# Kernel optimization log

Measured on AMD Instinct MI355X. Metric: run time of the kernel, lower is better.

## Reference

```python
import jax, jax.numpy as jnp
import numpy as np
from jax import lax

KS = 5            # patch kernel size
STRIDE = 4        # patch stride / scale ratio
SHIFTS = (2, 2)   # roll shifts before patch extraction
SOFTMAX_SCALE = 10.0
MID_CH = 64
BAND_HS = 8


def same_pad(x, k, s):
    """TensorFlow-style SAME padding for kernel k, stride s (NCHW)."""
    H, W = x.shape[-2], x.shape[-1]
    oh, ow = -(-H // s), -(-W // s)
    ph = max(0, (oh - 1) * s + k - H)
    pw = max(0, (ow - 1) * s + k - W)
    return jnp.pad(x, ((0, 0), (0, 0), (ph // 2, ph - ph // 2), (pw // 2, pw - pw // 2)))


def extract_patches(x, k, s, shifts):
    """torch.nn.Unfold equivalent with SAME padding and roll -> [N, L, C, k, k]."""
    x = same_pad(x, k, s)
    x = jnp.roll(x, shifts[0], axis=2)
    x = jnp.roll(x, shifts[1], axis=3)
    p = lax.conv_general_dilated_patches(
        x, (k, k), (s, s), 'VALID', dimension_numbers=('NCHW', 'OIHW', 'NCHW'))
    N, _, Hn, Wn = p.shape
    C = x.shape[1]
    # channel ordering is (C, kh, kw) channel-slowest, matching torch unfold
    return p.reshape(N, C, k, k, Hn * Wn).transpose(0, 4, 1, 2, 3)


def conv3(x, w, b):
    """3x3 conv, padding=1, bias + LeakyReLU(0.01) (BasicBlock)."""
    y = lax.conv_general_dilated(x, w, (1, 1), [(1, 1), (1, 1)],
                                 dimension_numbers=('NCHW', 'OIHW', 'NCHW'))
    return jax.nn.leaky_relu(y + b[None, :, None, None], 0.01)


def setup_inputs() -> dict:
    key = jax.random.key(0)
    ks = jax.random.split(key, 11)
    f32 = jnp.float32
    return {
        'ms':   jax.random.normal(ks[0], (2, BAND_HS, 96, 96), f32),
        'pan':  jax.random.normal(ks[1], (2, 1, 384, 384), f32),
        'pan2': jax.random.normal(ks[2], (2, 1, 96, 96), f32),
        'wq': jax.random.normal(ks[3], (MID_CH, 1, 3, 3), f32) * 0.1,
        'bq': jax.random.normal(ks[4], (MID_CH,), f32) * 0.02,
        'wk': jax.random.normal(ks[5], (MID_CH, 1, 3, 3), f32) * 0.1,
        'bk': jax.random.normal(ks[6], (MID_CH,), f32) * 0.02,
        'wv': jax.random.normal(ks[7], (BAND_HS, BAND_HS, 3, 3), f32) * 0.1,
        'bv': jax.random.normal(ks[8], (BAND_HS,), f32) * 0.02,
        'wr': jax.random.normal(ks[9], (BAND_HS, BAND_HS, 3, 3), f32) * 0.1,
        'br': jax.random.normal(ks[10], (BAND_HS,), f32) * 0.02,
    }


def reference(ms, pan, pan2, wq, bq, wk, bk, wv, bv, wr, br):
    k_fea = conv3(pan2, wk, bk)                       # [N, mid, h, w]
    q_fea = conv3(pan, wq, bq)                        # [N, mid, H, W]
    v_fea = conv3(ms, wv, bv)                         # [N, band, h, w]

    k_patch = extract_patches(k_fea, KS, STRIDE, SHIFTS)  # [N, L, mid, ks, ks]
    v_patch = extract_patches(v_fea, KS, STRIDE, SHIFTS)  # [N, L, band, ks, ks]

    def attend(q, kp, vp):
        # q: [mid, H, W]; kp: [L, mid, ks, ks]; vp: [L, band, ks, ks]
        norms = jnp.sqrt(jnp.sum(kp * kp, axis=(1, 2, 3)))      # per-patch L2 norms
        k0 = kp / jnp.max(norms)                                # global-max normalization
        q0 = same_pad(q[None], KS, STRIDE)                      # [1, mid, Hp, Wp]
        scores = lax.conv_general_dilated(
            q0, k0, (STRIDE, STRIDE), 'VALID',
            dimension_numbers=('NCHW', 'OIHW', 'NCHW'))          # [1, L, H', W']
        attn = jax.nn.softmax(scores * SOFTMAX_SCALE, axis=1)
        # conv_transpose2d(attn, vp, stride) == dilated conv with flipped, transposed kernel
        wT = jnp.flip(vp, (2, 3)).transpose(1, 0, 2, 3)          # [band, L, ks, ks]
        out = lax.conv_general_dilated(
            attn, wT, (1, 1), [(KS - 1, KS - 1)] * 2,
            lhs_dilation=(STRIDE, STRIDE),
            dimension_numbers=('NCHW', 'OIHW', 'NCHW'))          # [1, band, Ho, Wo]
        return out[0] / 6.0

    res = jax.vmap(attend)(q_fea, k_patch, v_patch)   # [N, band, Ho, Wo]
    return conv3(res, wr, br)
```

## Files before the change

kernel.cpp:

```cpp
#include <hip/hip_runtime.h>
#include <math.h>


typedef _Float16 f16;
typedef _Float16 f16x8 __attribute__((ext_vector_type(8)));
typedef float f32x4 __attribute__((ext_vector_type(4)));

namespace csa {
constexpr int NB   = 2;
constexpr int MID  = 64;
constexpr int BAND = 8;
constexpr int HK   = 96;
constexpr int HQ   = 384;
constexpr int HQP  = 385;
constexpr int XI   = 97;
constexpr int LN   = 24;
constexpr int L    = 576;
constexpr int LP   = 640;
constexpr int PS   = 96 * 96;
constexpr int KDIM = MID * 25;
constexpr int VDIM = BAND * 25;
constexpr int MV   = 256;
constexpr int HO   = 385;
constexpr size_t QPSN = (size_t)4 * HQP * XI * MID;

constexpr size_t align256(size_t x) { return (x + 255) & ~(size_t)255; }
constexpr size_t OFF_QPS  = 0;
constexpr size_t OFF_KCL  = align256(OFF_QPS + (size_t)NB*QPSN*2);
constexpr size_t OFF_VFEA = align256(OFF_KCL + (size_t)NB*HK*HK*MID*2);
constexpr size_t OFF_N2   = align256(OFF_VFEA + (size_t)NB*BAND*HK*HK*4);
constexpr size_t OFF_SC   = align256(OFF_N2   + (size_t)NB*L*4);
constexpr size_t OFF_KM   = align256(OFF_SC   + 256);
constexpr size_t OFF_VT   = align256(OFF_KM   + (size_t)NB*LP*KDIM*2);
constexpr size_t OFF_ST   = align256(OFF_VT   + (size_t)NB*MV*L*2);
constexpr size_t OFF_AT   = align256(OFF_ST   + (size_t)NB*PS*LP*4);
constexpr size_t OFF_D    = align256(OFF_AT   + (size_t)NB*PS*L*2);
constexpr size_t OFF_RES  = align256(OFF_D    + (size_t)NB*MV*PS*4);
}
using namespace csa;

__global__ __launch_bounds__(256) void csa_convq_ps(
    const float* __restrict__ in, const float* __restrict__ w,
    const float* __restrict__ b, f16* __restrict__ out) {
  int id = blockIdx.x * 256 + threadIdx.x;
  int total = NB * 4 * HQP * XI;
  if (id >= total) return;
  int xi = id % XI;
  int t = id / XI;
  int yp = t % HQP;
  t /= HQP;
  int f = t % 4;
  int n = t / 4;
  int xp = 4 * xi + f;
  f16* op = out + (size_t)id * MID;
  if (yp >= HQ || xp >= HQ) {
    f16x8 z = {0, 0, 0, 0, 0, 0, 0, 0};
#pragma unroll
    for (int c8 = 0; c8 < 8; ++c8) *(f16x8*)(op + c8 * 8) = z;
    return;
  }
  const float* ip = in + (size_t)n * HQ * HQ;
  float p[9];
#pragma unroll
  for (int dy = 0; dy < 3; ++dy)
#pragma unroll
    for (int dx = 0; dx < 3; ++dx) {
      int yy = yp + dy - 1, xx = xp + dx - 1;
      p[dy * 3 + dx] = (yy >= 0 && yy < HQ && xx >= 0 && xx < HQ)
                           ? ip[(size_t)yy * HQ + xx] : 0.f;
    }
#pragma unroll
  for (int c8 = 0; c8 < 8; ++c8) {
    f16x8 o;
#pragma unroll
    for (int e = 0; e < 8; ++e) {
      int co = c8 * 8 + e;
      float acc = b[co];
#pragma unroll
      for (int k = 0; k < 9; ++k) acc = fmaf(p[k], w[co * 9 + k], acc);
      o[e] = (f16)(acc > 0.f ? acc : 0.01f * acc);
    }
    *(f16x8*)(op + c8 * 8) = o;
  }
}

__global__ __launch_bounds__(256) void csa_conv_cl(
    const float* __restrict__ in, const float* __restrict__ w,
    const float* __restrict__ b, f16* __restrict__ out, int H) {
  int id = blockIdx.x * 256 + threadIdx.x;
  int total = NB * H * H;
  if (id >= total) return;
  int x = id % H;
  int t = id / H;
  int y = t % H;
  int n = t / H;
  f16* op = out + (size_t)id * MID;
  const float* ip = in + (size_t)n * H * H;
  float p[9];
#pragma unroll
  for (int dy = 0; dy < 3; ++dy)
#pragma unroll
    for (int dx = 0; dx < 3; ++dx) {
      int yy = y + dy - 1, xx = x + dx - 1;
      p[dy * 3 + dx] = (yy >= 0 && yy < H && xx >= 0 && xx < H)
                           ? ip[(size_t)yy * H + xx] : 0.f;
    }
#pragma unroll
  for (int c8 = 0; c8 < 8; ++c8) {
    f16x8 o;
#pragma unroll
    for (int e = 0; e < 8; ++e) {
      int co = c8 * 8 + e;
      float acc = b[co];
#pragma unroll
      for (int k = 0; k < 9; ++k) acc = fmaf(p[k], w[co * 9 + k], acc);
      o[e] = (f16)(acc > 0.f ? acc : 0.01f * acc);
    }
    *(f16x8*)(op + c8 * 8) = o;
  }
}

__global__ __launch_bounds__(256) void csa_conv3_8x8(
    const float* __restrict__ in, const float* __restrict__ w,
    const float* __restrict__ b, float* __restrict__ out, int H, int W) {
  int id = blockIdx.x * 256 + threadIdx.x;
  int total = NB * H * W;
  if (id >= total) return;
  int x = id % W;
  int t = id / W;
  int y = t % H;
  int n = t / H;
  const float* ip = in + (size_t)n * BAND * H * W;
  float p[BAND][9];
#pragma unroll
  for (int ci = 0; ci < BAND; ++ci)
#pragma unroll
    for (int dy = 0; dy < 3; ++dy)
#pragma unroll
      for (int dx = 0; dx < 3; ++dx) {
        int yy = y + dy - 1, xx = x + dx - 1;
        p[ci][dy * 3 + dx] = (yy >= 0 && yy < H && xx >= 0 && xx < W)
                                 ? ip[((size_t)ci * H + yy) * W + xx] : 0.f;
      }
  float* op = out + ((size_t)n * BAND * H + y) * W + x;
  for (int co = 0; co < BAND; ++co) {
    float acc = b[co];
#pragma unroll
    for (int ci = 0; ci < BAND; ++ci)
#pragma unroll
      for (int k = 0; k < 9; ++k)
        acc = fmaf(p[ci][k], w[(co * BAND + ci) * 9 + k], acc);
    acc = acc > 0.f ? acc : 0.01f * acc;
    op[(size_t)co * H * W] = acc;
  }
}

__global__ __launch_bounds__(256) void csa_build_patches(
    const f16* __restrict__ kcl, const float* __restrict__ v_fea,
    f16* __restrict__ Kmat, f16* __restrict__ Vt, float* __restrict__ n2) {
  int blk = blockIdx.x;
  int n = blk / LP;
  int l = blk % LP;
  int tid = threadIdx.x;
  f16* krow = Kmat + ((size_t)n * LP + l) * KDIM;
  if (l >= L) {
    f16x8 z = {0, 0, 0, 0, 0, 0, 0, 0};
    for (int ch = tid; ch < 200; ch += 256) *(f16x8*)(krow + ch * 8) = z;
    return;
  }
  int i = l / LN, j = l % LN;
  const f16* kn = kcl + (size_t)n * HK * HK * MID;
  float ss = 0.f;
  for (int ch = tid; ch < 200; ch += 256) {
    int khkw = ch >> 3;
    int c0 = (ch & 7) * 8;
    int kh = khkw / 5, kw = khkw % 5;
    int r = (4 * i + kh + 95) % 97;
    int cc = (4 * j + kw + 95) % 97;
    f16x8 v = {0, 0, 0, 0, 0, 0, 0, 0};
    if (r < HK && cc < HK)
      v = *(const f16x8*)(kn + ((size_t)r * HK + cc) * MID + c0);
#pragma unroll
    for (int e = 0; e < 8; ++e) {
      float fv = (float)v[e];
      ss += fv * fv;
    }
    *(f16x8*)(krow + ch * 8) = v;
  }
  for (int m = tid; m < MV; m += 256) {
    float v = 0.f;
    if (m < VDIM) {
      int kw = m % 5;
      int t = m / 5;
      int kh = t % 5;
      int c = t / 5;
      int r = (4 * i + kh + 95) % 97;
      int cc = (4 * j + kw + 95) % 97;
      v = (r < HK && cc < HK)
              ? v_fea[(((size_t)n * BAND + c) * HK + r) * HK + cc] : 0.f;
    }
    Vt[((size_t)n * MV + m) * L + l] = (f16)v;
  }
  __shared__ float red[256];
  red[tid] = ss;
  __syncthreads();
  for (int s = 128; s > 0; s >>= 1) {
    if (tid < s) red[tid] += red[tid + s];
    __syncthreads();
  }
  if (tid == 0) n2[n * L + l] = red[0];
}

__global__ __launch_bounds__(256) void csa_max_scale(
    const float* __restrict__ n2, float* __restrict__ scale) {
  int n = blockIdx.x;
  int tid = threadIdx.x;
  float m = 0.f;
  for (int l = tid; l < L; l += 256) m = fmaxf(m, n2[n * L + l]);
  __shared__ float red[256];
  red[tid] = m;
  __syncthreads();
  for (int s = 128; s > 0; s >>= 1) {
    if (tid < s) red[tid] = fmaxf(red[tid], red[tid + s]);
    __syncthreads();
  }
  if (tid == 0) scale[n] = 10.f / sqrtf(red[0]);
}

__device__ __forceinline__ void gl_lds16(const f16* g, f16* s) {
  __builtin_amdgcn_global_load_lds(
      (const __attribute__((address_space(1))) void*)g,
      (__attribute__((address_space(3))) void*)s, 16, 0, 0);
}

__global__ __launch_bounds__(256) void csa_gemm1(
    const f16* __restrict__ qps, const f16* __restrict__ Km,
    float* __restrict__ C) {
  __shared__ __attribute__((aligned(16))) f16 As[4096];
  __shared__ __attribute__((aligned(16))) f16 Bs[4096];
  const int tid = threadIdx.x;
  const int w = tid >> 6;
  const int l = tid & 63;
  const int q = l >> 4;
  const int r = l & 15;
  const int nb = blockIdx.z;
  qps += (size_t)nb * QPSN;
  Km += (size_t)nb * LP * KDIM;
  C += (size_t)nb * (size_t)PS * LP;
  const int bm = blockIdx.y * 128;
  const int bn = blockIdx.x * 128;
  const int wm = (w >> 1) * 64;
  const int wn = (w & 1) * 64;

  f32x4 acc[4][4];
#pragma unroll
  for (int i = 0; i < 4; ++i)
#pragma unroll
    for (int j = 0; j < 4; ++j) {
      f32x4 z = {0.f, 0.f, 0.f, 0.f};
      acc[i][j] = z;
    }

  const int pg0 = bm + w * 16;
  const int y0 = pg0 / 96, x0 = pg0 % 96;
  const int pg1 = pg0 + 64;
  const int y1 = pg1 / 96, x1 = pg1 % 96;
  const int la = r * MID + q * 8;

  const f16* gb0 = Km + (size_t)(bn + w * 16 + r) * KDIM + q * 8;
  const f16* gb1 = gb0 + (size_t)64 * KDIM;
  f16* lA0 = As + w * 512;
  f16* lA1 = As + 2048 + w * 512;
  f16* lB0 = Bs + w * 512;
  f16* lB1 = Bs + 2048 + w * 512;
  const int am = (w >> 1) * 4;
  const int bnn = (w & 1) * 4;

  int t = 0;
  for (int kh = 0; kh < 5; ++kh) {
    for (int kw = 0; kw < 5; ++kw) {
      const size_t u0 =
          (((size_t)(kw & 3) * HQP + (4 * y0 + kh)) * XI + x0 + (kw >> 2)) * MID;
      const size_t u1 =
          (((size_t)(kw & 3) * HQP + (4 * y1 + kh)) * XI + x1 + (kw >> 2)) * MID;
#pragma unroll
      for (int half = 0; half < 2; ++half, ++t) {
        const size_t oA = (size_t)half * 32 + la;
        const size_t oB = (size_t)t * 32;
        gl_lds16(qps + u0 + oA, lA0);
        gl_lds16(qps + u1 + oA, lA1);
        gl_lds16(gb0 + oB, lB0);
        gl_lds16(gb1 + oB, lB1);
        __syncthreads();
        f16x8 af[4], bf[4];
#pragma unroll
        for (int u = 0; u < 4; ++u) {
          af[u] = *(const f16x8*)&As[(am + u) * 512 + q * 128 + r * 8];
          bf[u] = *(const f16x8*)&Bs[(bnn + u) * 512 + q * 128 + r * 8];
        }
#pragma unroll
        for (int i = 0; i < 4; ++i)
#pragma unroll
          for (int j = 0; j < 4; ++j)
            acc[i][j] = __builtin_amdgcn_mfma_f32_16x16x32_f16(af[i], bf[j],
                                                               acc[i][j], 0, 0, 0);
        __syncthreads();
      }
    }
  }
  const int cn = bn + wn + r;
#pragma unroll
  for (int i = 0; i < 4; ++i) {
    int rm = bm + wm + i * 16 + q * 4;
#pragma unroll
    for (int j = 0; j < 4; ++j)
#pragma unroll
      for (int rr = 0; rr < 4; ++rr)
        C[(size_t)(rm + rr) * LP + cn + j * 16] = acc[i][j][rr];
  }
}

__global__ __launch_bounds__(256) void csa_gemm_f16(
    const f16* __restrict__ A, const f16* __restrict__ Bt,
    float* __restrict__ C, int M, int N, int K,
    size_t strideA, size_t strideB, size_t strideC) {
  __shared__ __attribute__((aligned(16))) f16 As[4096];
  __shared__ __attribute__((aligned(16))) f16 Bs[4096];
  const int tid = threadIdx.x;
  const int w = tid >> 6;
  const int l = tid & 63;
  const int q = l >> 4;
  const int r = l & 15;
  const int nb = blockIdx.z;
  A += (size_t)nb * strideA;
  Bt += (size_t)nb * strideB;
  C += (size_t)nb * strideC;
  const int bm = blockIdx.y * 128;
  const int bn = blockIdx.x * 128;
  const int wm = (w >> 1) * 64;
  const int wn = (w & 1) * 64;

  f32x4 acc[4][4];
#pragma unroll
  for (int i = 0; i < 4; ++i)
#pragma unroll
    for (int j = 0; j < 4; ++j) {
      f32x4 z = {0.f, 0.f, 0.f, 0.f};
      acc[i][j] = z;
    }

  const f16* ga0 = A + (size_t)(bm + w * 16 + r) * K + q * 8;
  const f16* ga1 = ga0 + (size_t)64 * K;
  const f16* gb0 = Bt + (size_t)(bn + w * 16 + r) * K + q * 8;
  const f16* gb1 = gb0 + (size_t)64 * K;
  f16* lA0 = As + w * 512;
  f16* lA1 = As + 2048 + w * 512;
  f16* lB0 = Bs + w * 512;
  f16* lB1 = Bs + 2048 + w * 512;
  const int am = (w >> 1) * 4;
  const int bnn = (w & 1) * 4;

  for (int k0 = 0; k0 < K; k0 += 32) {
    gl_lds16(ga0 + k0, lA0);
    gl_lds16(ga1 + k0, lA1);
    gl_lds16(gb0 + k0, lB0);
    gl_lds16(gb1 + k0, lB1);
    __syncthreads();
    f16x8 af[4], bf[4];
#pragma unroll
    for (int u = 0; u < 4; ++u) {
      af[u] = *(const f16x8*)&As[(am + u) * 512 + q * 128 + r * 8];
      bf[u] = *(const f16x8*)&Bs[(bnn + u) * 512 + q * 128 + r * 8];
    }
#pragma unroll
    for (int i = 0; i < 4; ++i)
#pragma unroll
      for (int j = 0; j < 4; ++j)
        acc[i][j] =
            __builtin_amdgcn_mfma_f32_16x16x32_f16(af[i], bf[j], acc[i][j], 0, 0, 0);
    __syncthreads();
  }

  const int cn = bn + wn + r;
#pragma unroll
  for (int i = 0; i < 4; ++i) {
    int rm = bm + wm + i * 16 + q * 4;
#pragma unroll
    for (int j = 0; j < 4; ++j)
#pragma unroll
      for (int rr = 0; rr < 4; ++rr)
        C[(size_t)(rm + rr) * N + cn + j * 16] = acc[i][j][rr];
  }
}

__global__ __launch_bounds__(256) void csa_softmax(
    const float* __restrict__ scoresT, const float* __restrict__ scale,
    f16* __restrict__ attnT) {
  const int wv = threadIdx.x >> 6;
  const int lane = threadIdx.x & 63;
  const int p = blockIdx.x * 4 + wv;
  const int n = blockIdx.y;
  const float sc = scale[n];
  const float* row = scoresT + ((size_t)n * PS + p) * LP;
  float v[9];
  float m = -1e30f;
#pragma unroll
  for (int j = 0; j < 9; ++j) {
    v[j] = row[lane + j * 64] * sc;
    m = fmaxf(m, v[j]);
  }
#pragma unroll
  for (int off = 32; off > 0; off >>= 1) m = fmaxf(m, __shfl_xor(m, off));
  float e[9], s = 0.f;
#pragma unroll
  for (int j = 0; j < 9; ++j) {
    e[j] = __expf(v[j] - m);
    s += e[j];
  }
#pragma unroll
  for (int off = 32; off > 0; off >>= 1) s += __shfl_xor(s, off);
  const float inv = 1.f / s;
  f16* orow = attnT + ((size_t)n * PS + p) * L;
#pragma unroll
  for (int j = 0; j < 9; ++j) orow[lane + j * 64] = (f16)(e[j] * inv);
}

__global__ __launch_bounds__(256) void csa_gather(
    const float* __restrict__ D, float* __restrict__ res) {
  int id = blockIdx.x * 256 + threadIdx.x;
  if (id >= NB * BAND * HO * HO) return;
  int ox = id % HO;
  int t = id / HO;
  int oy = t % HO;
  t = t / HO;
  int co = t % BAND;
  int n = t / BAND;
  const float* Dn = D + (size_t)n * MV * PS;
  float s = 0.f;
  int kh0 = oy & 3;
  int kw0 = ox & 3;
  for (int kh = kh0; kh < 5; kh += 4) {
    int y = (oy - kh) >> 2;
    if (y < 0 || y >= 96) continue;
    for (int kw = kw0; kw < 5; kw += 4) {
      int x = (ox - kw) >> 2;
      if (x < 0 || x >= 96) continue;
      s += Dn[(size_t)(co * 25 + kh * 5 + kw) * PS + y * 96 + x];
    }
  }
  res[id] = s * (1.f / 6.f);
}

extern "C" void kernel_launch(void* const* d_in, const int* in_sizes, int n_in,
                              void* d_out, int out_size, void* d_ws,
                              size_t ws_size, hipStream_t stream) {
  const float* ms   = (const float*)d_in[0];
  const float* pan  = (const float*)d_in[1];
  const float* pan2 = (const float*)d_in[2];
  const float* wq = (const float*)d_in[3];
  const float* bq = (const float*)d_in[4];
  const float* wk = (const float*)d_in[5];
  const float* bk = (const float*)d_in[6];
  const float* wv = (const float*)d_in[7];
  const float* bv = (const float*)d_in[8];
  const float* wr = (const float*)d_in[9];
  const float* br = (const float*)d_in[10];
  float* out = (float*)d_out;

  char* ws = (char*)d_ws;
  f16*   qps   = (f16*)(ws + OFF_QPS);
  f16*   kcl   = (f16*)(ws + OFF_KCL);
  float* v_fea = (float*)(ws + OFF_VFEA);
  float* n2    = (float*)(ws + OFF_N2);
  float* scale = (float*)(ws + OFF_SC);
  f16*   Kmat  = (f16*)(ws + OFF_KM);
  f16*   Vt    = (f16*)(ws + OFF_VT);
  float* scoT  = (float*)(ws + OFF_ST);
  f16*   attnT = (f16*)(ws + OFF_AT);
  float* Dm    = (float*)(ws + OFF_D);
  float* res   = (float*)(ws + OFF_RES);

  dim3 b256(256);
  csa_convq_ps<<<dim3((NB * 4 * HQP * XI + 255) / 256), b256, 0, stream>>>(
      pan, wq, bq, qps);
  csa_conv_cl<<<dim3((NB * HK * HK + 255) / 256), b256, 0, stream>>>(
      pan2, wk, bk, kcl, HK);
  csa_conv3_8x8<<<dim3((NB * HK * HK + 255) / 256), b256, 0, stream>>>(
      ms, wv, bv, v_fea, HK, HK);
  csa_build_patches<<<dim3(NB * LP), b256, 0, stream>>>(kcl, v_fea, Kmat, Vt,
                                                        n2);
  csa_max_scale<<<dim3(NB), b256, 0, stream>>>(n2, scale);

  csa_gemm1<<<dim3(LP / 128, PS / 128, NB), b256, 0, stream>>>(qps, Kmat,
                                                               scoT);

  csa_softmax<<<dim3(PS / 4, NB), b256, 0, stream>>>(scoT, scale, attnT);

  csa_gemm_f16<<<dim3(PS / 128, MV / 128, NB), b256, 0, stream>>>(
      Vt, attnT, Dm, MV, PS, L,
      (size_t)MV * L, (size_t)PS * L, (size_t)MV * PS);

  csa_gather<<<dim3((NB * BAND * HO * HO + 255) / 256), b256, 0, stream>>>(
      Dm, res);
  csa_conv3_8x8<<<dim3((NB * HO * HO + 255) / 256), b256, 0, stream>>>(
      res, wr, br, out, HO, HO);
}
```

Measured before the change: 278.8 us.

## Triple-buffer GEMM LDS staging with async prefetch, XCD-aware block remap, compact scores

Both MFMA GEMM kernels now use a three-stage LDS ring. Global-to-LDS loads for tile t+2 are issued before computing tile t, with a single vmcnt wait and barrier per step replacing two syncthreads. Workgroup indices are remapped so consecutive logical tiles land on the same XCD, improving L2 reuse across the eight chiplets. The scores matrix is stored with row stride 576 instead of padded 640, with column-guarded writes, which cuts write and softmax read traffic at the cost of triple the LDS footprint.

```diff
diff --git a/kernel.cpp b/kernel.cpp
--- a/kernel.cpp
+++ b/kernel.cpp
@@ -236,19 +236,25 @@
 __global__ __launch_bounds__(256) void csa_gemm1(
     const f16* __restrict__ qps, const f16* __restrict__ Km,
     float* __restrict__ C) {
-  __shared__ __attribute__((aligned(16))) f16 As[4096];
-  __shared__ __attribute__((aligned(16))) f16 Bs[4096];
+  __shared__ __attribute__((aligned(16))) f16 As[3 * 4096];
+  __shared__ __attribute__((aligned(16))) f16 Bs[3 * 4096];
   const int tid = threadIdx.x;
   const int w = tid >> 6;
   const int l = tid & 63;
   const int q = l >> 4;
   const int r = l & 15;
-  const int nb = blockIdx.z;
+
+  const int flat = blockIdx.x + 5 * (blockIdx.y + 72 * blockIdx.z);
+  const int logical = (flat & 7) * 90 + (flat >> 3);
+  const int bx = logical % 5;
+  const int by = (logical / 5) % 72;
+  const int nb = logical / 360;
+
   qps += (size_t)nb * QPSN;
   Km += (size_t)nb * LP * KDIM;
-  C += (size_t)nb * (size_t)PS * LP;
-  const int bm = blockIdx.y * 128;
-  const int bn = blockIdx.x * 128;
+  C += (size_t)nb * (size_t)PS * L;
+  const int bm = by * 128;
+  const int bn = bx * 128;
   const int wm = (w >> 1) * 64;
   const int wn = (w & 1) * 64;
 
@@ -269,54 +275,77 @@
 
   const f16* gb0 = Km + (size_t)(bn + w * 16 + r) * KDIM + q * 8;
   const f16* gb1 = gb0 + (size_t)64 * KDIM;
-  f16* lA0 = As + w * 512;
-  f16* lA1 = As + 2048 + w * 512;
-  f16* lB0 = Bs + w * 512;
-  f16* lB1 = Bs + 2048 + w * 512;
   const int am = (w >> 1) * 4;
   const int bnn = (w & 1) * 4;
 
-  int t = 0;
-  for (int kh = 0; kh < 5; ++kh) {
-    for (int kw = 0; kw < 5; ++kw) {
-      const size_t u0 =
-          (((size_t)(kw & 3) * HQP + (4 * y0 + kh)) * XI + x0 + (kw >> 2)) * MID;
-      const size_t u1 =
-          (((size_t)(kw & 3) * HQP + (4 * y1 + kh)) * XI + x1 + (kw >> 2)) * MID;
-#pragma unroll
-      for (int half = 0; half < 2; ++half, ++t) {
-        const size_t oA = (size_t)half * 32 + la;
-        const size_t oB = (size_t)t * 32;
-        gl_lds16(qps + u0 + oA, lA0);
-        gl_lds16(qps + u1 + oA, lA1);
-        gl_lds16(gb0 + oB, lB0);
-        gl_lds16(gb1 + oB, lB1);
-        __syncthreads();
-        f16x8 af[4], bf[4];
-#pragma unroll
-        for (int u = 0; u < 4; ++u) {
-          af[u] = *(const f16x8*)&As[(am + u) * 512 + q * 128 + r * 8];
-          bf[u] = *(const f16x8*)&Bs[(bnn + u) * 512 + q * 128 + r * 8];
-        }
-#pragma unroll
-        for (int i = 0; i < 4; ++i)
-#pragma unroll
-          for (int j = 0; j < 4; ++j)
-            acc[i][j] = __builtin_amdgcn_mfma_f32_16x16x32_f16(af[i], bf[j],
-                                                               acc[i][j], 0, 0, 0);
-        __syncthreads();
-      }
-    }
-  }
+  auto stage = [&](int t, int bi) {
+    f16* bA = As + bi * 4096;
+    f16* bB = Bs + bi * 4096;
+    const int kh = t / 10;
+    const int rem = t - kh * 10;
+    const int kw = rem >> 1;
+    const int half = rem & 1;
+    const size_t u0 =
+        (((size_t)(kw & 3) * HQP + (4 * y0 + kh)) * XI + x0 + (kw >> 2)) * MID;
+    const size_t u1 =
+        (((size_t)(kw & 3) * HQP + (4 * y1 + kh)) * XI + x1 + (kw >> 2)) * MID;
+    const size_t oA = (size_t)half * 32 + la;
+    gl_lds16(qps + u0 + oA, bA + w * 512);
+    gl_lds16(qps + u1 + oA, bA + 2048 + w * 512);
+    gl_lds16(gb0 + (size_t)t * 32, bB + w * 512);
+    gl_lds16(gb1 + (size_t)t * 32, bB + 2048 + w * 512);
+  };
+  auto compute = [&](int bi) {
+    const f16* bA = As + bi * 4096;
+    const f16* bB = Bs + bi * 4096;
+    f16x8 af[4], bf[4];
+#pragma unroll
+    for (int u = 0; u < 4; ++u) {
+      af[u] = *(const f16x8*)&bA[(am + u) * 512 + q * 128 + r * 8];
+      bf[u] = *(const f16x8*)&bB[(bnn + u) * 512 + q * 128 + r * 8];
+    }
+#pragma unroll
+    for (int i = 0; i < 4; ++i)
+#pragma unroll
+      for (int j = 0; j < 4; ++j)
+        acc[i][j] = __builtin_amdgcn_mfma_f32_16x16x32_f16(af[i], bf[j],
+                                                           acc[i][j], 0, 0, 0);
+  };
+
+  stage(0, 0);
+  stage(1, 1);
+  int bi = 0;
+  for (int t = 0; t < 48; ++t) {
+    asm volatile("s_waitcnt vmcnt(4)" ::: "memory");
+    __builtin_amdgcn_s_barrier();
+    __builtin_amdgcn_sched_barrier(0);
+    stage(t + 2, bi == 0 ? 2 : bi - 1);
+    compute(bi);
+    bi = (bi == 2) ? 0 : bi + 1;
+  }
+  asm volatile("s_waitcnt vmcnt(4)" ::: "memory");
+  __builtin_amdgcn_s_barrier();
+  __builtin_amdgcn_sched_barrier(0);
+  compute(bi);
+  bi = (bi == 2) ? 0 : bi + 1;
+  asm volatile("s_waitcnt vmcnt(0)" ::: "memory");
+  __builtin_amdgcn_s_barrier();
+  __builtin_amdgcn_sched_barrier(0);
+  compute(bi);
+
   const int cn = bn + wn + r;
 #pragma unroll
   for (int i = 0; i < 4; ++i) {
     int rm = bm + wm + i * 16 + q * 4;
 #pragma unroll
-    for (int j = 0; j < 4; ++j)
-#pragma unroll
-      for (int rr = 0; rr < 4; ++rr)
-        C[(size_t)(rm + rr) * LP + cn + j * 16] = acc[i][j][rr];
+    for (int j = 0; j < 4; ++j) {
+      int c = cn + j * 16;
+      if (c < L) {
+#pragma unroll
+        for (int rr = 0; rr < 4; ++rr)
+          C[(size_t)(rm + rr) * L + c] = acc[i][j][rr];
+      }
+    }
   }
 }
 
@@ -324,19 +353,28 @@
     const f16* __restrict__ A, const f16* __restrict__ Bt,
     float* __restrict__ C, int M, int N, int K,
     size_t strideA, size_t strideB, size_t strideC) {
-  __shared__ __attribute__((aligned(16))) f16 As[4096];
-  __shared__ __attribute__((aligned(16))) f16 Bs[4096];
+  __shared__ __attribute__((aligned(16))) f16 As[3 * 4096];
+  __shared__ __attribute__((aligned(16))) f16 Bs[3 * 4096];
   const int tid = threadIdx.x;
   const int w = tid >> 6;
   const int l = tid & 63;
   const int q = l >> 4;
   const int r = l & 15;
-  const int nb = blockIdx.z;
+
+  const int gx = gridDim.x, gy = gridDim.y;
+  const int nwg = gx * gy * gridDim.z;
+  const int chunk = nwg >> 3;
+  const int flat = blockIdx.x + gx * (blockIdx.y + gy * blockIdx.z);
+  const int logical = (flat & 7) * chunk + (flat >> 3);
+  const int my = logical % gy;
+  const int nx = (logical / gy) % gx;
+  const int nb = logical / (gy * gx);
+
   A += (size_t)nb * strideA;
   Bt += (size_t)nb * strideB;
   C += (size_t)nb * strideC;
-  const int bm = blockIdx.y * 128;
-  const int bn = blockIdx.x * 128;
+  const int bm = my * 128;
+  const int bn = nx * 128;
   const int wm = (w >> 1) * 64;
   const int wn = (w & 1) * 64;
 
@@ -353,24 +391,26 @@
   const f16* ga1 = ga0 + (size_t)64 * K;
   const f16* gb0 = Bt + (size_t)(bn + w * 16 + r) * K + q * 8;
   const f16* gb1 = gb0 + (size_t)64 * K;
-  f16* lA0 = As + w * 512;
-  f16* lA1 = As + 2048 + w * 512;
-  f16* lB0 = Bs + w * 512;
-  f16* lB1 = Bs + 2048 + w * 512;
   const int am = (w >> 1) * 4;
   const int bnn = (w & 1) * 4;
 
-  for (int k0 = 0; k0 < K; k0 += 32) {
-    gl_lds16(ga0 + k0, lA0);
-    gl_lds16(ga1 + k0, lA1);
-    gl_lds16(gb0 + k0, lB0);
-    gl_lds16(gb1 + k0, lB1);
-    __syncthreads();
+  auto stage = [&](int t, int bi) {
+    f16* bA = As + bi * 4096;
+    f16* bB = Bs + bi * 4096;
+    const size_t k0 = (size_t)t * 32;
+    gl_lds16(ga0 + k0, bA + w * 512);
+    gl_lds16(ga1 + k0, bA + 2048 + w * 512);
+    gl_lds16(gb0 + k0, bB + w * 512);
+    gl_lds16(gb1 + k0, bB + 2048 + w * 512);
+  };
+  auto compute = [&](int bi) {
+    const f16* bA = As + bi * 4096;
+    const f16* bB = Bs + bi * 4096;
     f16x8 af[4], bf[4];
 #pragma unroll
     for (int u = 0; u < 4; ++u) {
-      af[u] = *(const f16x8*)&As[(am + u) * 512 + q * 128 + r * 8];
-      bf[u] = *(const f16x8*)&Bs[(bnn + u) * 512 + q * 128 + r * 8];
+      af[u] = *(const f16x8*)&bA[(am + u) * 512 + q * 128 + r * 8];
+      bf[u] = *(const f16x8*)&bB[(bnn + u) * 512 + q * 128 + r * 8];
     }
 #pragma unroll
     for (int i = 0; i < 4; ++i)
@@ -378,8 +418,29 @@
       for (int j = 0; j < 4; ++j)
         acc[i][j] =
             __builtin_amdgcn_mfma_f32_16x16x32_f16(af[i], bf[j], acc[i][j], 0, 0, 0);
-    __syncthreads();
-  }
+  };
+
+  const int NT = K >> 5;
+  stage(0, 0);
+  stage(1, 1);
+  int bi = 0;
+  for (int t = 0; t + 2 < NT; ++t) {
+    asm volatile("s_waitcnt vmcnt(4)" ::: "memory");
+    __builtin_amdgcn_s_barrier();
+    __builtin_amdgcn_sched_barrier(0);
+    stage(t + 2, bi == 0 ? 2 : bi - 1);
+    compute(bi);
+    bi = (bi == 2) ? 0 : bi + 1;
+  }
+  asm volatile("s_waitcnt vmcnt(4)" ::: "memory");
+  __builtin_amdgcn_s_barrier();
+  __builtin_amdgcn_sched_barrier(0);
+  compute(bi);
+  bi = (bi == 2) ? 0 : bi + 1;
+  asm volatile("s_waitcnt vmcnt(0)" ::: "memory");
+  __builtin_amdgcn_s_barrier();
+  __builtin_amdgcn_sched_barrier(0);
+  compute(bi);
 
   const int cn = bn + wn + r;
 #pragma unroll
@@ -401,7 +462,7 @@
   const int p = blockIdx.x * 4 + wv;
   const int n = blockIdx.y;
   const float sc = scale[n];
-  const float* row = scoresT + ((size_t)n * PS + p) * LP;
+  const float* row = scoresT + ((size_t)n * PS + p) * L;
   float v[9];
   float m = -1e30f;
 #pragma unroll
```

Result: faster. 273.3 us (-2.0%).

## Replace LDS-staged GEMMs with register double-buffered direct loads and XCD-aware block remap

Applied to the files above, without the earlier changes.

Both MFMA GEMMs stop staging tiles through LDS with global_load_lds and barriers. Each wave now loads its f16x8 fragments straight from global memory into registers, double-buffered so the next K-step's loads overlap the current MFMAs. Block indices are remapped so consecutive logical tiles land on the same XCD, aiming for better L2 reuse. The scores buffer is narrowed from padded LP to L columns with a bounds check, and gemm2 uses 64-row tiles for more blocks. The risks are redundant global loads with no LDS sharing across waves, and the remap constants being hardcoded to the grid shape.

```diff
diff --git a/kernel.cpp b/kernel.cpp
--- a/kernel.cpp
+++ b/kernel.cpp
@@ -227,28 +227,26 @@
   if (tid == 0) scale[n] = 10.f / sqrtf(red[0]);
 }
 
-__device__ __forceinline__ void gl_lds16(const f16* g, f16* s) {
-  __builtin_amdgcn_global_load_lds(
-      (const __attribute__((address_space(1))) void*)g,
-      (__attribute__((address_space(3))) void*)s, 16, 0, 0);
-}
-
 __global__ __launch_bounds__(256) void csa_gemm1(
     const f16* __restrict__ qps, const f16* __restrict__ Km,
     float* __restrict__ C) {
-  __shared__ __attribute__((aligned(16))) f16 As[4096];
-  __shared__ __attribute__((aligned(16))) f16 Bs[4096];
   const int tid = threadIdx.x;
   const int w = tid >> 6;
   const int l = tid & 63;
   const int q = l >> 4;
   const int r = l & 15;
-  const int nb = blockIdx.z;
+
+  const int flat = blockIdx.x + 5 * (blockIdx.y + 72 * blockIdx.z);
+  const int logical = (flat & 7) * 90 + (flat >> 3);
+  const int bx = logical % 5;
+  const int by = (logical / 5) % 72;
+  const int nb = logical / 360;
+
   qps += (size_t)nb * QPSN;
   Km += (size_t)nb * LP * KDIM;
-  C += (size_t)nb * (size_t)PS * LP;
-  const int bm = blockIdx.y * 128;
-  const int bn = blockIdx.x * 128;
+  C += (size_t)nb * (size_t)PS * L;
+  const int bm = by * 128;
+  const int bn = bx * 128;
   const int wm = (w >> 1) * 64;
   const int wn = (w & 1) * 64;
 
@@ -261,135 +259,145 @@
       acc[i][j] = z;
     }
 
-  const int pg0 = bm + w * 16;
-  const int y0 = pg0 / 96, x0 = pg0 % 96;
-  const int pg1 = pg0 + 64;
-  const int y1 = pg1 / 96, x1 = pg1 % 96;
-  const int la = r * MID + q * 8;
-
-  const f16* gb0 = Km + (size_t)(bn + w * 16 + r) * KDIM + q * 8;
-  const f16* gb1 = gb0 + (size_t)64 * KDIM;
-  f16* lA0 = As + w * 512;
-  f16* lA1 = As + 2048 + w * 512;
-  f16* lB0 = Bs + w * 512;
-  f16* lB1 = Bs + 2048 + w * 512;
-  const int am = (w >> 1) * 4;
-  const int bnn = (w & 1) * 4;
-
-  int t = 0;
-  for (int kh = 0; kh < 5; ++kh) {
-    for (int kw = 0; kw < 5; ++kw) {
-      const size_t u0 =
-          (((size_t)(kw & 3) * HQP + (4 * y0 + kh)) * XI + x0 + (kw >> 2)) * MID;
-      const size_t u1 =
-          (((size_t)(kw & 3) * HQP + (4 * y1 + kh)) * XI + x1 + (kw >> 2)) * MID;
-#pragma unroll
-      for (int half = 0; half < 2; ++half, ++t) {
-        const size_t oA = (size_t)half * 32 + la;
-        const size_t oB = (size_t)t * 32;
-        gl_lds16(qps + u0 + oA, lA0);
-        gl_lds16(qps + u1 + oA, lA1);
-        gl_lds16(gb0 + oB, lB0);
-        gl_lds16(gb1 + oB, lB1);
-        __syncthreads();
-        f16x8 af[4], bf[4];
-#pragma unroll
-        for (int u = 0; u < 4; ++u) {
-          af[u] = *(const f16x8*)&As[(am + u) * 512 + q * 128 + r * 8];
-          bf[u] = *(const f16x8*)&Bs[(bnn + u) * 512 + q * 128 + r * 8];
-        }
-#pragma unroll
-        for (int i = 0; i < 4; ++i)
-#pragma unroll
-          for (int j = 0; j < 4; ++j)
-            acc[i][j] = __builtin_amdgcn_mfma_f32_16x16x32_f16(af[i], bf[j],
-                                                               acc[i][j], 0, 0, 0);
-        __syncthreads();
-      }
-    }
-  }
+  const f16* pA[4];
+#pragma unroll
+  for (int u = 0; u < 4; ++u) {
+    const int p0 = bm + wm + 16 * u;
+    const int yu = p0 / 96, x0u = p0 % 96;
+    pA[u] = qps + ((size_t)(4 * yu) * XI + x0u + r) * MID + q * 8;
+  }
+  const f16* pB[4];
+#pragma unroll
+  for (int u = 0; u < 4; ++u)
+    pB[u] = Km + (size_t)(bn + wn + 16 * u + r) * KDIM + q * 8;
+
+  auto loadt = [&](int t, f16x8 av[4], f16x8 bv[4]) {
+    const int khkw = t >> 1, half = t & 1;
+    const int kh = khkw / 5, kw = khkw % 5;
+    const size_t dA =
+        (((size_t)(kw & 3) * HQP + kh) * XI + (kw >> 2)) * MID + half * 32;
+#pragma unroll
+    for (int u = 0; u < 4; ++u) {
+      av[u] = *(const f16x8*)(pA[u] + dA);
+      bv[u] = *(const f16x8*)(pB[u] + t * 32);
+    }
+  };
+  auto mfmas = [&](const f16x8 av[4], const f16x8 bv[4]) {
+#pragma unroll
+    for (int i = 0; i < 4; ++i)
+#pragma unroll
+      for (int j = 0; j < 4; ++j)
+        acc[i][j] = __builtin_amdgcn_mfma_f32_16x16x32_f16(av[i], bv[j],
+                                                           acc[i][j], 0, 0, 0);
+  };
+
+  f16x8 a0[4], b0[4], a1[4], b1[4];
+  loadt(0, a0, b0);
+#pragma unroll
+  for (int t = 0; t < 48; t += 2) {
+    loadt(t + 1, a1, b1);
+    mfmas(a0, b0);
+    loadt(t + 2, a0, b0);
+    mfmas(a1, b1);
+  }
+  loadt(49, a1, b1);
+  mfmas(a0, b0);
+  mfmas(a1, b1);
+
   const int cn = bn + wn + r;
 #pragma unroll
   for (int i = 0; i < 4; ++i) {
     int rm = bm + wm + i * 16 + q * 4;
 #pragma unroll
-    for (int j = 0; j < 4; ++j)
-#pragma unroll
-      for (int rr = 0; rr < 4; ++rr)
-        C[(size_t)(rm + rr) * LP + cn + j * 16] = acc[i][j][rr];
-  }
-}
-
-__global__ __launch_bounds__(256) void csa_gemm_f16(
-    const f16* __restrict__ A, const f16* __restrict__ Bt,
-    float* __restrict__ C, int M, int N, int K,
-    size_t strideA, size_t strideB, size_t strideC) {
-  __shared__ __attribute__((aligned(16))) f16 As[4096];
-  __shared__ __attribute__((aligned(16))) f16 Bs[4096];
+    for (int j = 0; j < 4; ++j) {
+      int c = cn + j * 16;
+      if (c < L) {
+#pragma unroll
+        for (int rr = 0; rr < 4; ++rr)
+          C[(size_t)(rm + rr) * L + c] = acc[i][j][rr];
+      }
+    }
+  }
+}
+
+__global__ __launch_bounds__(256) void csa_gemm2(
+    const f16* __restrict__ Vt, const f16* __restrict__ At,
+    float* __restrict__ D) {
   const int tid = threadIdx.x;
   const int w = tid >> 6;
   const int l = tid & 63;
   const int q = l >> 4;
   const int r = l & 15;
-  const int nb = blockIdx.z;
-  A += (size_t)nb * strideA;
-  Bt += (size_t)nb * strideB;
-  C += (size_t)nb * strideC;
-  const int bm = blockIdx.y * 128;
-  const int bn = blockIdx.x * 128;
-  const int wm = (w >> 1) * 64;
+
+  const int flat = blockIdx.x + 72 * (blockIdx.y + 4 * blockIdx.z);
+  const int logical = (flat & 7) * 72 + (flat >> 3);
+  const int nx = logical % 72;
+  const int my = (logical / 72) % 4;
+  const int nb = logical / 288;
+
+  const f16* A = Vt + (size_t)nb * MV * L;
+  const f16* Bt = At + (size_t)nb * (size_t)PS * L;
+  float* C = D + (size_t)nb * (size_t)MV * PS;
+  const int bm = my * 64;
+  const int bn = nx * 128;
+  const int wm = (w >> 1) * 32;
   const int wn = (w & 1) * 64;
 
-  f32x4 acc[4][4];
-#pragma unroll
-  for (int i = 0; i < 4; ++i)
+  f32x4 acc[2][4];
+#pragma unroll
+  for (int i = 0; i < 2; ++i)
 #pragma unroll
     for (int j = 0; j < 4; ++j) {
       f32x4 z = {0.f, 0.f, 0.f, 0.f};
       acc[i][j] = z;
     }
 
-  const f16* ga0 = A + (size_t)(bm + w * 16 + r) * K + q * 8;
-  const f16* ga1 = ga0 + (size_t)64 * K;
-  const f16* gb0 = Bt + (size_t)(bn + w * 16 + r) * K + q * 8;
-  const f16* gb1 = gb0 + (size_t)64 * K;
-  f16* lA0 = As + w * 512;
-  f16* lA1 = As + 2048 + w * 512;
-  f16* lB0 = Bs + w * 512;
-  f16* lB1 = Bs + 2048 + w * 512;
-  const int am = (w >> 1) * 4;
-  const int bnn = (w & 1) * 4;
-
-  for (int k0 = 0; k0 < K; k0 += 32) {
-    gl_lds16(ga0 + k0, lA0);
-    gl_lds16(ga1 + k0, lA1);
-    gl_lds16(gb0 + k0, lB0);
-    gl_lds16(gb1 + k0, lB1);
-    __syncthreads();
-    f16x8 af[4], bf[4];
-#pragma unroll
-    for (int u = 0; u < 4; ++u) {
-      af[u] = *(const f16x8*)&As[(am + u) * 512 + q * 128 + r * 8];
-      bf[u] = *(const f16x8*)&Bs[(bnn + u) * 512 + q * 128 + r * 8];
-    }
-#pragma unroll
-    for (int i = 0; i < 4; ++i)
+  const f16* pA[2];
+#pragma unroll
+  for (int u = 0; u < 2; ++u)
+    pA[u] = A + (size_t)(bm + wm + 16 * u + r) * L + q * 8;
+  const f16* pB[4];
+#pragma unroll
+  for (int u = 0; u < 4; ++u)
+    pB[u] = Bt + (size_t)(bn + wn + 16 * u + r) * L + q * 8;
+
+  auto loadt = [&](int t, f16x8 av[2], f16x8 bv[4]) {
+#pragma unroll
+    for (int u = 0; u < 2; ++u) av[u] = *(const f16x8*)(pA[u] + t * 32);
+#pragma unroll
+    for (int u = 0; u < 4; ++u) bv[u] = *(const f16x8*)(pB[u] + t * 32);
+  };
+  auto mfmas = [&](const f16x8 av[2], const f16x8 bv[4]) {
+#pragma unroll
+    for (int i = 0; i < 2; ++i)
 #pragma unroll
       for (int j = 0; j < 4; ++j)
-        acc[i][j] =
-            __builtin_amdgcn_mfma_f32_16x16x32_f16(af[i], bf[j], acc[i][j], 0, 0, 0);
-    __syncthreads();
-  }
+        acc[i][j] = __builtin_amdgcn_mfma_f32_16x16x32_f16(av[i], bv[j],
+                                                           acc[i][j], 0, 0, 0);
+  };
+
+  f16x8 a0[2], b0[4], a1[2], b1[4];
+  loadt(0, a0, b0);
+#pragma unroll
+  for (int t = 0; t < 16; t += 2) {
+    loadt(t + 1, a1, b1);
+    mfmas(a0, b0);
+    loadt(t + 2, a0, b0);
+    mfmas(a1, b1);
+  }
+  loadt(17, a1, b1);
+  mfmas(a0, b0);
+  mfmas(a1, b1);
 
   const int cn = bn + wn + r;
 #pragma unroll
-  for (int i = 0; i < 4; ++i) {
+  for (int i = 0; i < 2; ++i) {
     int rm = bm + wm + i * 16 + q * 4;
 #pragma unroll
     for (int j = 0; j < 4; ++j)
 #pragma unroll
       for (int rr = 0; rr < 4; ++rr)
-        C[(size_t)(rm + rr) * N + cn + j * 16] = acc[i][j][rr];
+        C[(size_t)(rm + rr) * PS + cn + j * 16] = acc[i][j][rr];
   }
 }
 
@@ -401,7 +409,7 @@
   const int p = blockIdx.x * 4 + wv;
   const int n = blockIdx.y;
   const float sc = scale[n];
-  const float* row = scoresT + ((size_t)n * PS + p) * LP;
+  const float* row = scoresT + ((size_t)n * PS + p) * L;
   float v[9];
   float m = -1e30f;
 #pragma unroll
@@ -496,9 +504,7 @@
 
   csa_softmax<<<dim3(PS / 4, NB), b256, 0, stream>>>(scoT, scale, attnT);
 
-  csa_gemm_f16<<<dim3(PS / 128, MV / 128, NB), b256, 0, stream>>>(
-      Vt, attnT, Dm, MV, PS, L,
-      (size_t)MV * L, (size_t)PS * L, (size_t)MV * PS);
+  csa_gemm2<<<dim3(PS / 128, MV / 64, NB), b256, 0, stream>>>(Vt, attnT, Dm);
 
   csa_gather<<<dim3((NB * BAND * HO * HO + 255) / 256), b256, 0, stream>>>(
       Dm, res);
```

New measurement: 357.0 us. +28.0%, slower.
